# Optimization experiments

Measured on AMD Instinct MI355X. Metric: run time of the kernel, lower is better.

Reference implementation:

```python
import jax, jax.numpy as jnp
import numpy as np

B, T, F, H = 2048, 512, 64, 16


def setup_inputs() -> dict:
    key = jax.random.key(0)
    ks = jax.random.split(key, 10)
    s = 0.05  # small init so relu-activated LSTM state stays bounded over 512 steps
    return {
        "x": jax.random.normal(ks[0], (B, T, F), dtype=jnp.float32),
        "Wx": jax.random.normal(ks[1], (F, 4 * H), dtype=jnp.float32) * s,
        "Wh": jax.random.normal(ks[2], (H, 4 * H), dtype=jnp.float32) * s,
        "b": jnp.zeros((4 * H,), dtype=jnp.float32),
        "W2": jax.random.normal(ks[3], (H, 8), dtype=jnp.float32) * 0.3,
        "b2": jnp.zeros((8,), dtype=jnp.float32),
        "W3": jax.random.normal(ks[4], (8, 4), dtype=jnp.float32) * 0.3,
        "b3": jnp.zeros((4,), dtype=jnp.float32),
        "Wo": jax.random.normal(ks[5], (4, 1), dtype=jnp.float32) * 0.3,
        "bo": jnp.zeros((1,), dtype=jnp.float32),
    }


def reference(x, Wx, Wh, b, W2, b2, W3, b3, Wo, bo):
    # Keras LSTM, gate order [i, f, c(g), o]; recurrent_activation=sigmoid,
    # activation=relu (applied to candidate g AND to cell state in h = o*relu(c)).
    # Precompute input projections for all timesteps, scan only the recurrence.
    xz = jnp.einsum('btf,fg->btg', x, Wx) + b  # [B, T, 4H]
    h0 = jnp.zeros((x.shape[0], H), dtype=x.dtype)
    c0 = jnp.zeros((x.shape[0], H), dtype=x.dtype)

    def step(carry, xz_t):
        h, c = carry
        z = xz_t + h @ Wh  # [B, 4H]
        i = jax.nn.sigmoid(z[:, 0 * H:1 * H])
        f = jax.nn.sigmoid(z[:, 1 * H:2 * H])
        g = jax.nn.relu(z[:, 2 * H:3 * H])
        o = jax.nn.sigmoid(z[:, 3 * H:4 * H])
        c_new = f * c + i * g
        h_new = o * jax.nn.relu(c_new)
        return (h_new, c_new), None

    (h_T, _), _ = jax.lax.scan(step, (h0, c0), jnp.swapaxes(xz, 0, 1))
    # Dropout layers are identity at inference (training=False).
    x2 = jax.nn.relu(h_T @ W2 + b2)
    x3 = jax.nn.relu(x2 @ W3 + b3)
    return jax.nn.sigmoid(x3 @ Wo + bo)  # [B, 1]
```

## Files before the change

kernel.cpp:

```cpp
#include <hip/hip_runtime.h>
#include <stdint.h>

#define Bdim 2048
#define Tdim 512
#define NBLK (Tdim / 16)

#define TSTRIDE 68
#define RSTRIDE (16 * TSTRIDE + 8)
#define BUFD (4 * RSTRIDE)
#define HSTRIDE 20

typedef __attribute__((ext_vector_type(8))) short bf16x8;
typedef __attribute__((ext_vector_type(4))) float f32x4;

__device__ __forceinline__ uint16_t f2bf(float f) {
    union { float f; uint32_t u; } v; v.f = f;
    uint32_t r = v.u + 0x7fffu + ((v.u >> 16) & 1u);
    return (uint16_t)(r >> 16);
}
__device__ __forceinline__ float sigmoidf(float z) {
    return __builtin_amdgcn_rcpf(1.0f + __expf(-z));
}

__global__ __launch_bounds__(64, 1) void lstm_fused(
    const float* __restrict__ x, const float* __restrict__ Wx,
    const float* __restrict__ bias, const float* __restrict__ Wh,
    const float* __restrict__ W2, const float* __restrict__ b2,
    const float* __restrict__ W3, const float* __restrict__ b3,
    const float* __restrict__ Wo, const float* __restrict__ bo,
    float* __restrict__ out)
{
    __shared__ __align__(16) float zbuf[2 * BUFD];
    __shared__ __align__(16) float hbuf[4 * HSTRIDE];

    const int lane = threadIdx.x;
    const int l15  = lane & 15;
    const int quad = lane >> 4;
    const int r    = quad;
    const int j    = l15;
    const int b0   = blockIdx.x * 4;

    float wi[16], wf[16], wg[16], wo_[16];
    #pragma unroll
    for (int k = 0; k < 16; ++k) {
        const float* row = Wh + (size_t)k * 64 + j;
        wi[k]  = row[0];
        wf[k]  = row[16];
        wg[k]  = row[32];
        wo_[k] = row[48];
    }

    bf16x8 wxf[4][2];
    #pragma unroll
    for (int nt = 0; nt < 4; ++nt)
        #pragma unroll
        for (int kc = 0; kc < 2; ++kc)
            #pragma unroll
            for (int jj = 0; jj < 8; ++jj)
                wxf[nt][kc][jj] =
                    (short)f2bf(Wx[(size_t)(kc * 32 + quad * 8 + jj) * 64 + nt * 16 + l15]);

    float bv[4];
    #pragma unroll
    for (int nt = 0; nt < 4; ++nt) bv[nt] = bias[nt * 16 + l15];

    float4 xn[4][2][2];
    auto load_tile = [&](int t0) {
        #pragma unroll
        for (int rr = 0; rr < 4; ++rr) {
            const float* p = x + ((size_t)(b0 + rr) * Tdim + t0 + l15) * 64 + quad * 8;
            xn[rr][0][0] = *(const float4*)(p);
            xn[rr][0][1] = *(const float4*)(p + 4);
            xn[rr][1][0] = *(const float4*)(p + 32);
            xn[rr][1][1] = *(const float4*)(p + 36);
        }
    };

    auto project = [&](int q) {
        #pragma unroll
        for (int rr = 0; rr < 4; ++rr) {
            bf16x8 af[2];
            #pragma unroll
            for (int kc = 0; kc < 2; ++kc) {
                const float4 p0 = xn[rr][kc][0], p1 = xn[rr][kc][1];
                af[kc][0] = (short)f2bf(p0.x); af[kc][1] = (short)f2bf(p0.y);
                af[kc][2] = (short)f2bf(p0.z); af[kc][3] = (short)f2bf(p0.w);
                af[kc][4] = (short)f2bf(p1.x); af[kc][5] = (short)f2bf(p1.y);
                af[kc][6] = (short)f2bf(p1.z); af[kc][7] = (short)f2bf(p1.w);
            }
            f32x4 acc[4];
            #pragma unroll
            for (int nt = 0; nt < 4; ++nt) {
                f32x4 a = {bv[nt], bv[nt], bv[nt], bv[nt]};
                a = __builtin_amdgcn_mfma_f32_16x16x32_bf16(af[0], wxf[nt][0], a, 0, 0, 0);
                a = __builtin_amdgcn_mfma_f32_16x16x32_bf16(af[1], wxf[nt][1], a, 0, 0, 0);
                acc[nt] = a;
            }
            #pragma unroll
            for (int reg = 0; reg < 4; ++reg) {
                float4 w4;
                w4.x = acc[0][reg]; w4.y = acc[1][reg];
                w4.z = acc[2][reg]; w4.w = acc[3][reg];
                *(float4*)&zbuf[q * BUFD + rr * RSTRIDE +
                                (quad * 4 + reg) * TSTRIDE + l15 * 4] = w4;
            }
        }
    };

    const int zoff = r * RSTRIDE + j * 4;
    auto readz = [&](int q, int t) -> float4 {
        return *(const float4*)&zbuf[q * BUFD + zoff + t * TSTRIDE];
    };

    load_tile(0);
    project(0);
    load_tile(16);

    float c = 0.f, h = 0.f;
    float hk[16];
    #pragma unroll
    for (int k = 0; k < 16; ++k) hk[k] = 0.f;
    float4 zc = readz(0, 0);

    for (int n = 0; n < NBLK; ++n) {
        const int p = n & 1;
        if (n + 1 < NBLK) {
            project(p ^ 1);
            if (n + 2 < NBLK) load_tile((n + 2) * 16);
        }
        #pragma unroll
        for (int u = 0; u < 16; ++u) {
            float4 zn = (u < 15) ? readz(p, u + 1) : readz(p ^ 1, 0);

            float zi = zc.x, zf = zc.y, zg = zc.z, zo = zc.w;
            #pragma unroll
            for (int k = 0; k < 16; ++k) {
                zi = fmaf(hk[k], wi[k],  zi);
                zf = fmaf(hk[k], wf[k],  zf);
                zg = fmaf(hk[k], wg[k],  zg);
                zo = fmaf(hk[k], wo_[k], zo);
            }
            const float i_ = sigmoidf(zi);
            const float f_ = sigmoidf(zf);
            const float o_ = sigmoidf(zo);
            const float g_ = fmaxf(zg, 0.f);
            c = fmaf(f_, c, i_ * g_);
            h = o_ * fmaxf(c, 0.f);

            hbuf[r * HSTRIDE + j] = h;
            const float4* hb = (const float4*)&hbuf[r * HSTRIDE];
            float4 h0 = hb[0], h1 = hb[1], h2 = hb[2], h3 = hb[3];
            hk[0]  = h0.x; hk[1]  = h0.y; hk[2]  = h0.z; hk[3]  = h0.w;
            hk[4]  = h1.x; hk[5]  = h1.y; hk[6]  = h1.z; hk[7]  = h1.w;
            hk[8]  = h2.x; hk[9]  = h2.y; hk[10] = h2.z; hk[11] = h2.w;
            hk[12] = h3.x; hk[13] = h3.y; hk[14] = h3.z; hk[15] = h3.w;

            zc = zn;
        }
    }

    if (j == 0) {
        float x2[8];
        #pragma unroll
        for (int k = 0; k < 8; ++k) {
            float s = b2[k];
            #pragma unroll
            for (int q = 0; q < 16; ++q) s = fmaf(hk[q], W2[(size_t)q * 8 + k], s);
            x2[k] = fmaxf(s, 0.f);
        }
        float x3[4];
        #pragma unroll
        for (int m = 0; m < 4; ++m) {
            float s = b3[m];
            #pragma unroll
            for (int k = 0; k < 8; ++k) s = fmaf(x2[k], W3[(size_t)k * 4 + m], s);
            x3[m] = fmaxf(s, 0.f);
        }
        float s = bo[0];
        #pragma unroll
        for (int m = 0; m < 4; ++m) s = fmaf(x3[m], Wo[m], s);
        out[b0 + r] = sigmoidf(s);
    }
}

extern "C" void kernel_launch(void* const* d_in, const int* in_sizes, int n_in,
                              void* d_out, int out_size, void* d_ws, size_t ws_size,
                              hipStream_t stream) {
    const float* x  = (const float*)d_in[0];
    const float* Wx = (const float*)d_in[1];
    const float* Wh = (const float*)d_in[2];
    const float* bb = (const float*)d_in[3];
    const float* W2 = (const float*)d_in[4];
    const float* b2 = (const float*)d_in[5];
    const float* W3 = (const float*)d_in[6];
    const float* b3 = (const float*)d_in[7];
    const float* Wo = (const float*)d_in[8];
    const float* bo = (const float*)d_in[9];

    lstm_fused<<<Bdim / 4, 64, 0, stream>>>(x, Wx, bb, Wh, W2, b2, W3, b3,
                                            Wo, bo, (float*)d_out);
}
```

Before: 407.2 us.

## Assign one batch row per wavefront, one gate column per lane

Each wavefront now processes one batch element instead of four. Each of the 64 lanes computes one gate pre-activation (a 16-term dot product split into two accumulator chains) and the four gates are exchanged with shuffles. The grid grows to 2048 blocks and launch bounds allow two waves per SIMD, shortening the serial dependency chain per step and raising occupancy. In exchange, MFMA projection work per block is used at one quarter of a tile, and the shuffles add latency on the recurrent critical path.

```diff
diff --git a/kernel.cpp b/kernel.cpp
--- a/kernel.cpp
+++ b/kernel.cpp
@@ -6,9 +6,7 @@
 #define NBLK (Tdim / 16)
 
 #define TSTRIDE 68
-#define RSTRIDE (16 * TSTRIDE + 8)
-#define BUFD (4 * RSTRIDE)
-#define HSTRIDE 20
+#define BUFD (16 * TSTRIDE)
 
 typedef __attribute__((ext_vector_type(8))) short bf16x8;
 typedef __attribute__((ext_vector_type(4))) float f32x4;
@@ -22,7 +20,7 @@
     return __builtin_amdgcn_rcpf(1.0f + __expf(-z));
 }
 
-__global__ __launch_bounds__(64, 1) void lstm_fused(
+__global__ __launch_bounds__(64, 2) void lstm_fused(
     const float* __restrict__ x, const float* __restrict__ Wx,
     const float* __restrict__ bias, const float* __restrict__ Wh,
     const float* __restrict__ W2, const float* __restrict__ b2,
@@ -31,24 +29,16 @@
     float* __restrict__ out)
 {
     __shared__ __align__(16) float zbuf[2 * BUFD];
-    __shared__ __align__(16) float hbuf[4 * HSTRIDE];
+    __shared__ __align__(16) float hbuf[16];
 
     const int lane = threadIdx.x;
     const int l15  = lane & 15;
     const int quad = lane >> 4;
-    const int r    = quad;
-    const int j    = l15;
-    const int b0   = blockIdx.x * 4;
+    const int b    = blockIdx.x;
 
-    float wi[16], wf[16], wg[16], wo_[16];
+    float w[16];
     #pragma unroll
-    for (int k = 0; k < 16; ++k) {
-        const float* row = Wh + (size_t)k * 64 + j;
-        wi[k]  = row[0];
-        wf[k]  = row[16];
-        wg[k]  = row[32];
-        wo_[k] = row[48];
-    }
+    for (int k = 0; k < 16; ++k) w[k] = Wh[(size_t)k * 64 + lane];
 
     bf16x8 wxf[4][2];
     #pragma unroll
@@ -64,52 +54,45 @@
     #pragma unroll
     for (int nt = 0; nt < 4; ++nt) bv[nt] = bias[nt * 16 + l15];
 
-    float4 xn[4][2][2];
+    float4 xn[4];
     auto load_tile = [&](int t0) {
+        const float* p = x + ((size_t)b * Tdim + t0 + l15) * 64 + quad * 8;
+        xn[0] = *(const float4*)(p);
+        xn[1] = *(const float4*)(p + 4);
+        xn[2] = *(const float4*)(p + 32);
+        xn[3] = *(const float4*)(p + 36);
+    };
+
+    auto project = [&](int q) {
+        bf16x8 af[2];
         #pragma unroll
-        for (int rr = 0; rr < 4; ++rr) {
-            const float* p = x + ((size_t)(b0 + rr) * Tdim + t0 + l15) * 64 + quad * 8;
-            xn[rr][0][0] = *(const float4*)(p);
-            xn[rr][0][1] = *(const float4*)(p + 4);
-            xn[rr][1][0] = *(const float4*)(p + 32);
-            xn[rr][1][1] = *(const float4*)(p + 36);
+        for (int kc = 0; kc < 2; ++kc) {
+            const float4 p0 = xn[kc * 2], p1 = xn[kc * 2 + 1];
+            af[kc][0] = (short)f2bf(p0.x); af[kc][1] = (short)f2bf(p0.y);
+            af[kc][2] = (short)f2bf(p0.z); af[kc][3] = (short)f2bf(p0.w);
+            af[kc][4] = (short)f2bf(p1.x); af[kc][5] = (short)f2bf(p1.y);
+            af[kc][6] = (short)f2bf(p1.z); af[kc][7] = (short)f2bf(p1.w);
+        }
+        f32x4 acc[4];
+        #pragma unroll
+        for (int nt = 0; nt < 4; ++nt) {
+            f32x4 a = {bv[nt], bv[nt], bv[nt], bv[nt]};
+            a = __builtin_amdgcn_mfma_f32_16x16x32_bf16(af[0], wxf[nt][0], a, 0, 0, 0);
+            a = __builtin_amdgcn_mfma_f32_16x16x32_bf16(af[1], wxf[nt][1], a, 0, 0, 0);
+            acc[nt] = a;
+        }
+        #pragma unroll
+        for (int reg = 0; reg < 4; ++reg) {
+            float4 w4;
+            w4.x = acc[0][reg]; w4.y = acc[1][reg];
+            w4.z = acc[2][reg]; w4.w = acc[3][reg];
+            *(float4*)&zbuf[q * BUFD + (quad * 4 + reg) * TSTRIDE + l15 * 4] = w4;
         }
     };
 
-    auto project = [&](int q) {
-        #pragma unroll
-        for (int rr = 0; rr < 4; ++rr) {
-            bf16x8 af[2];
-            #pragma unroll
-            for (int kc = 0; kc < 2; ++kc) {
-                const float4 p0 = xn[rr][kc][0], p1 = xn[rr][kc][1];
-                af[kc][0] = (short)f2bf(p0.x); af[kc][1] = (short)f2bf(p0.y);
-                af[kc][2] = (short)f2bf(p0.z); af[kc][3] = (short)f2bf(p0.w);
-                af[kc][4] = (short)f2bf(p1.x); af[kc][5] = (short)f2bf(p1.y);
-                af[kc][6] = (short)f2bf(p1.z); af[kc][7] = (short)f2bf(p1.w);
-            }
-            f32x4 acc[4];
-            #pragma unroll
-            for (int nt = 0; nt < 4; ++nt) {
-                f32x4 a = {bv[nt], bv[nt], bv[nt], bv[nt]};
-                a = __builtin_amdgcn_mfma_f32_16x16x32_bf16(af[0], wxf[nt][0], a, 0, 0, 0);
-                a = __builtin_amdgcn_mfma_f32_16x16x32_bf16(af[1], wxf[nt][1], a, 0, 0, 0);
-                acc[nt] = a;
-            }
-            #pragma unroll
-            for (int reg = 0; reg < 4; ++reg) {
-                float4 w4;
-                w4.x = acc[0][reg]; w4.y = acc[1][reg];
-                w4.z = acc[2][reg]; w4.w = acc[3][reg];
-                *(float4*)&zbuf[q * BUFD + rr * RSTRIDE +
-                                (quad * 4 + reg) * TSTRIDE + l15 * 4] = w4;
-            }
-        }
-    };
-
-    const int zoff = r * RSTRIDE + j * 4;
-    auto readz = [&](int q, int t) -> float4 {
-        return *(const float4*)&zbuf[q * BUFD + zoff + t * TSTRIDE];
+    const int zoff = l15 * 4 + quad;
+    auto readz = [&](int q, int t) -> float {
+        return zbuf[q * BUFD + t * TSTRIDE + zoff];
     };
 
     load_tile(0);
@@ -120,7 +103,7 @@
     float hk[16];
     #pragma unroll
     for (int k = 0; k < 16; ++k) hk[k] = 0.f;
-    float4 zc = readz(0, 0);
+    float zc = readz(0, 0);
 
     for (int n = 0; n < NBLK; ++n) {
         const int p = n & 1;
@@ -130,25 +113,28 @@
         }
         #pragma unroll
         for (int u = 0; u < 16; ++u) {
-            float4 zn = (u < 15) ? readz(p, u + 1) : readz(p ^ 1, 0);
+            float zn = (u < 15) ? readz(p, u + 1) : readz(p ^ 1, 0);
 
-            float zi = zc.x, zf = zc.y, zg = zc.z, zo = zc.w;
+            float a0 = zc, a1 = 0.f;
             #pragma unroll
-            for (int k = 0; k < 16; ++k) {
-                zi = fmaf(hk[k], wi[k],  zi);
-                zf = fmaf(hk[k], wf[k],  zf);
-                zg = fmaf(hk[k], wg[k],  zg);
-                zo = fmaf(hk[k], wo_[k], zo);
+            for (int k = 0; k < 8; ++k) {
+                a0 = fmaf(hk[k],     w[k],     a0);
+                a1 = fmaf(hk[k + 8], w[k + 8], a1);
             }
-            const float i_ = sigmoidf(zi);
-            const float f_ = sigmoidf(zf);
-            const float o_ = sigmoidf(zo);
-            const float g_ = fmaxf(zg, 0.f);
+            const float z = a0 + a1;
+            const float sig = sigmoidf(z);
+            const float a = (quad == 2) ? fmaxf(z, 0.f) : sig;
+
+            const float i_ = __shfl(a, l15);
+            const float f_ = __shfl(a, l15 + 16);
+            const float g_ = __shfl(a, l15 + 32);
+            const float o_ = __shfl(a, l15 + 48);
+
             c = fmaf(f_, c, i_ * g_);
             h = o_ * fmaxf(c, 0.f);
 
-            hbuf[r * HSTRIDE + j] = h;
-            const float4* hb = (const float4*)&hbuf[r * HSTRIDE];
+            hbuf[l15] = h;
+            const float4* hb = (const float4*)hbuf;
             float4 h0 = hb[0], h1 = hb[1], h2 = hb[2], h3 = hb[3];
             hk[0]  = h0.x; hk[1]  = h0.y; hk[2]  = h0.z; hk[3]  = h0.w;
             hk[4]  = h1.x; hk[5]  = h1.y; hk[6]  = h1.z; hk[7]  = h1.w;
@@ -159,7 +145,7 @@
         }
     }
 
-    if (j == 0) {
+    if (lane == 0) {
         float x2[8];
         #pragma unroll
         for (int k = 0; k < 8; ++k) {
@@ -179,7 +165,7 @@
         float s = bo[0];
         #pragma unroll
         for (int m = 0; m < 4; ++m) s = fmaf(x3[m], Wo[m], s);
-        out[b0 + r] = sigmoidf(s);
+        out[b] = sigmoidf(s);
     }
 }
 
@@ -197,6 +183,6 @@
     const float* Wo = (const float*)d_in[8];
     const float* bo = (const float*)d_in[9];
 
-    lstm_fused<<<Bdim / 4, 64, 0, stream>>>(x, Wx, bb, Wh, W2, b2, W3, b3,
-                                            Wo, bo, (float*)d_out);
+    lstm_fused<<<Bdim, 64, 0, stream>>>(x, Wx, bb, Wh, W2, b2, W3, b3,
+                                        Wo, bo, (float*)d_out);
 }
```

After: 388.1 us. -4.7%, faster.
